# Optimization experiments

Measured on AMD Instinct MI355X. Metric: run time of the kernel, lower is better.

## Reference

```python
import jax, jax.numpy as jnp
import numpy as np

S, N, M, D = 4, 4096, 4096, 128
NEG = -1e30
EPS = 1e-12


def setup_inputs() -> dict:
    key = jax.random.key(0)
    k1, k2, k3 = jax.random.split(key, 3)
    art = jax.random.normal(k1, (S, N, D), dtype=jnp.float32)
    ref = jax.random.normal(k2, (S, M, D), dtype=jnp.float32)
    pos_mask = jax.random.randint(k3, (S, N, M), 0, 2).astype(jnp.bool_)
    log_temperature = jnp.log(jnp.asarray(0.01, dtype=jnp.float32))
    return {"art": art, "ref": ref, "pos_mask": pos_mask, "log_temperature": log_temperature}


def _l2norm(x):
    # F.normalize: x / max(||x||, eps)
    n = jnp.sqrt(jnp.sum(x * x, axis=-1, keepdims=True))
    return x / jnp.maximum(n, EPS)


def reference(art, ref, pos_mask, log_temperature):
    temp = jnp.exp(log_temperature)
    a = _l2norm(art)                                   # [S,N,D]
    r = _l2norm(ref)                                   # [S,M,D]
    logits = jnp.einsum("snd,smd->snm", a, r) / temp   # [S,N,M]

    den = jax.nn.logsumexp(logits, axis=-1)                              # [S,N]
    num = jax.nn.logsumexp(jnp.where(pos_mask, logits, NEG), axis=-1)    # [S,N]

    n_pos = jnp.sum(pos_mask, axis=-1)                 # [S,N]
    n_ref = logits.shape[-1]
    valid = (n_pos > 0) & (n_ref > n_pos)              # skip anchors with 0 pos or all pos

    per_anchor = den - num                             # -(num - den)
    cnt = jnp.sum(valid, axis=-1)                      # [S]
    stem_loss = jnp.sum(jnp.where(valid, per_anchor, 0.0), axis=-1) / jnp.maximum(cnt, 1)
    stem_valid = cnt > 0
    loss = jnp.sum(jnp.where(stem_valid, stem_loss, 0.0)) / jnp.maximum(jnp.sum(stem_valid), 1)
    return loss
```

## Files before the change

kernel.cpp:

```cpp
#include <hip/hip_runtime.h>
#include <hip/hip_bf16.h>
#include <math.h>

#define S_ 4
#define N_ 4096
#define M_ 4096
#define D_ 128
#define NEG_ (-1e30f)
#define CH_ 4
#define MCH_ (M_ / CH_)

typedef __bf16 bf16x8 __attribute__((ext_vector_type(8)));
typedef float f32x4 __attribute__((ext_vector_type(4)));

__device__ __forceinline__ unsigned short f2bf(float f) {
    unsigned u = __float_as_uint(f);
    unsigned r = (u + 0x7FFFu + ((u >> 16) & 1u)) >> 16;
    return (unsigned short)r;
}

__global__ void nrm_rows_kernel(const float* __restrict__ art, const float* __restrict__ ref,
                                unsigned short* __restrict__ an, unsigned short* __restrict__ rn) {
    const int w = threadIdx.x >> 6;
    const int lane = threadIdx.x & 63;
    const int row = blockIdx.x * 4 + w;
    const bool is_art = row < S_ * N_;
    const float* src = is_art ? (art + (size_t)row * D_)
                              : (ref + (size_t)(row - S_ * N_) * D_);
    unsigned short* dst = is_art ? (an + (size_t)row * D_)
                                 : (rn + (size_t)(row - S_ * N_) * D_);
    const float2 v = *reinterpret_cast<const float2*>(src + lane * 2);
    float ss = v.x * v.x + v.y * v.y;
#pragma unroll
    for (int off = 1; off < 64; off <<= 1) ss += __shfl_xor(ss, off);
    const float scale = 1.0f / fmaxf(sqrtf(ss), 1e-12f);
    unsigned pack = (unsigned)f2bf(v.x * scale) | ((unsigned)f2bf(v.y * scale) << 16);
    *reinterpret_cast<unsigned*>(dst + lane * 2) = pack;
}

__global__ __launch_bounds__(256, 6) void infonce_main_kernel(
    const unsigned short* __restrict__ an, const unsigned short* __restrict__ rn,
    const void* __restrict__ maskp, const float* __restrict__ logtemp,
    float4* __restrict__ part4, float* __restrict__ partn) {

    const int bid = blockIdx.x;
    const int swz = (bid & 7) * 256 + (bid >> 3);
    const int ch = swz >> 9;
    const int s = (swz >> 7) & 3;
    const int nblk = swz & 127;
    const int n_base = nblk * 32;

    const int tid = threadIdx.x;
    const int w = tid >> 6;
    const int lane = tid & 63;
    const int nsub = w & 1;
    const int msub = w >> 1;
    const int n16 = n_base + nsub * 16;
    const int lrow = lane & 15;
    const int lgrp = lane >> 4;
    const float inv_temp = __expf(-logtemp[0]);

    const unsigned probe = ((const unsigned*)maskp)[lane];
    const bool mask_is_byte = (__ballot(probe > 1u) != 0ull);

    bf16x8 bfr[4];
    const unsigned short* abase = an + ((size_t)(s * N_ + n16 + lrow)) * D_ + lgrp * 8;
#pragma unroll
    for (int kc = 0; kc < 4; ++kc)
        bfr[kc] = *reinterpret_cast<const bf16x8*>(abase + kc * 32);

    float dmax = NEG_, dsum = 0.f, nmax = NEG_, nsum = 0.f;
    int npos = 0;

    const int m_begin = ch * MCH_ + msub * (MCH_ / 2);
    const unsigned short* rbase = rn + ((size_t)(s * M_ + m_begin + lrow)) * D_ + lgrp * 8;
    const size_t mrow = ((size_t)(s * N_ + n16 + lrow)) * M_;

    for (int it = 0; it < (MCH_ / 2) / 32; ++it) {
        const int t0 = it * 2, t1 = t0 + 1;
        const int m0a = m_begin + t0 * 16 + lgrp * 4;
        const int m0b = m_begin + t1 * 16 + lgrp * 4;
        int pm[8];
        if (mask_is_byte) {
            const uchar4 ma = *reinterpret_cast<const uchar4*>((const unsigned char*)maskp + mrow + m0a);
            const uchar4 mb = *reinterpret_cast<const uchar4*>((const unsigned char*)maskp + mrow + m0b);
            pm[0] = ma.x; pm[1] = ma.y; pm[2] = ma.z; pm[3] = ma.w;
            pm[4] = mb.x; pm[5] = mb.y; pm[6] = mb.z; pm[7] = mb.w;
        } else {
            const int4 ma = *reinterpret_cast<const int4*>((const int*)maskp + mrow + m0a);
            const int4 mb = *reinterpret_cast<const int4*>((const int*)maskp + mrow + m0b);
            pm[0] = ma.x; pm[1] = ma.y; pm[2] = ma.z; pm[3] = ma.w;
            pm[4] = mb.x; pm[5] = mb.y; pm[6] = mb.z; pm[7] = mb.w;
        }
        f32x4 acc0 = {0.f, 0.f, 0.f, 0.f}, acc1 = {0.f, 0.f, 0.f, 0.f};
        const unsigned short* rp0 = rbase + (size_t)t0 * 16 * D_;
        const unsigned short* rp1 = rbase + (size_t)t1 * 16 * D_;
#pragma unroll
        for (int kc = 0; kc < 4; ++kc) {
            acc0 = __builtin_amdgcn_mfma_f32_16x16x32_bf16(
                *reinterpret_cast<const bf16x8*>(rp0 + kc * 32), bfr[kc], acc0, 0, 0, 0);
            acc1 = __builtin_amdgcn_mfma_f32_16x16x32_bf16(
                *reinterpret_cast<const bf16x8*>(rp1 + kc * 32), bfr[kc], acc1, 0, 0, 0);
        }
        float l[8];
#pragma unroll
        for (int i = 0; i < 4; ++i) { l[i] = acc0[i] * inv_temp; l[i + 4] = acc1[i] * inv_temp; }
        float tmax = fmaxf(fmaxf(fmaxf(l[0], l[1]), fmaxf(l[2], l[3])),
                           fmaxf(fmaxf(l[4], l[5]), fmaxf(l[6], l[7])));
        float nmx = fmaxf(dmax, tmax);
        float e = __expf(dmax - nmx) * dsum;
#pragma unroll
        for (int i = 0; i < 8; ++i) e += __expf(l[i] - nmx);
        dsum = e; dmax = nmx;
        float sm[8];
#pragma unroll
        for (int i = 0; i < 8; ++i) sm[i] = pm[i] ? l[i] : NEG_;
        float tmax2 = fmaxf(fmaxf(fmaxf(sm[0], sm[1]), fmaxf(sm[2], sm[3])),
                            fmaxf(fmaxf(sm[4], sm[5]), fmaxf(sm[6], sm[7])));
        float nmx2 = fmaxf(nmax, tmax2);
        float e2 = __expf(nmax - nmx2) * nsum;
#pragma unroll
        for (int i = 0; i < 8; ++i) e2 += __expf(sm[i] - nmx2);
        nsum = e2; nmax = nmx2;
#pragma unroll
        for (int i = 0; i < 8; ++i) npos += (pm[i] != 0);
    }

#pragma unroll
    for (int off = 16; off < 64; off <<= 1) {
        float odm = __shfl_xor(dmax, off), ods = __shfl_xor(dsum, off);
        float onm = __shfl_xor(nmax, off), ons = __shfl_xor(nsum, off);
        int onp = __shfl_xor(npos, off);
        float nm = fmaxf(dmax, odm);
        dsum = dsum * __expf(dmax - nm) + ods * __expf(odm - nm);
        dmax = nm;
        float nm2 = fmaxf(nmax, onm);
        nsum = nsum * __expf(nmax - nm2) + ons * __expf(onm - nm2);
        nmax = nm2;
        npos += onp;
    }

    __shared__ float lds[4][16][5];
    if (lane < 16) {
        lds[w][lane][0] = dmax; lds[w][lane][1] = dsum;
        lds[w][lane][2] = nmax; lds[w][lane][3] = nsum;
        lds[w][lane][4] = (float)npos;
    }
    __syncthreads();

    if (w == 0 && lane < 32) {
        const int wsub = lane >> 4;
        const int ni = lane & 15;
        float adm = lds[wsub][ni][0], ads = lds[wsub][ni][1];
        float anm = lds[wsub][ni][2], ans = lds[wsub][ni][3];
        float apc = lds[wsub][ni][4];
        float bdm = lds[wsub + 2][ni][0], bds = lds[wsub + 2][ni][1];
        float bnm = lds[wsub + 2][ni][2], bns = lds[wsub + 2][ni][3];
        float bpc = lds[wsub + 2][ni][4];
        float dm = fmaxf(adm, bdm);
        float ds = ads * __expf(adm - dm) + bds * __expf(bdm - dm);
        float nm = fmaxf(anm, bnm);
        float ns = ans * __expf(anm - nm) + bns * __expf(bnm - nm);
        const int ag = s * N_ + n_base + wsub * 16 + ni;
        part4[ag * CH_ + ch] = make_float4(dm, ds, nm, ns);
        partn[ag * CH_ + ch] = apc + bpc;
    }
}

__global__ void reduce_kernel(const float4* __restrict__ part4, const float* __restrict__ partn,
                              float* __restrict__ accum) {
    const int a = blockIdx.x * 256 + threadIdx.x;
    const int s = a >> 12;
    const int w = threadIdx.x >> 6;
    const int lane = threadIdx.x & 63;
    float dm = NEG_, ds = 0.f, nm = NEG_, ns = 0.f, np = 0.f;
#pragma unroll
    for (int ch = 0; ch < CH_; ++ch) {
        const float4 p = part4[a * CH_ + ch];
        const float pn = partn[a * CH_ + ch];
        float m2 = fmaxf(dm, p.x);
        ds = ds * __expf(dm - m2) + p.y * __expf(p.x - m2);
        dm = m2;
        float m3 = fmaxf(nm, p.z);
        ns = ns * __expf(nm - m3) + p.w * __expf(p.z - m3);
        nm = m3;
        np += pn;
    }
    const int npi = (int)np;
    const bool valid = (npi > 0) && (npi < M_);
    float pa = valid ? ((dm + __logf(ds)) - (nm + __logf(ns))) : 0.f;
    float cv = valid ? 1.f : 0.f;
#pragma unroll
    for (int off = 1; off < 64; off <<= 1) {
        pa += __shfl_xor(pa, off);
        cv += __shfl_xor(cv, off);
    }
    __shared__ float sp[4], sc[4];
    if (lane == 0) { sp[w] = pa; sc[w] = cv; }
    __syncthreads();
    if (threadIdx.x == 0) {
        atomicAdd(&accum[s * 2 + 0], sp[0] + sp[1] + sp[2] + sp[3]);
        atomicAdd(&accum[s * 2 + 1], sc[0] + sc[1] + sc[2] + sc[3]);
    }
}

__global__ void finalize_kernel(const float* __restrict__ accum, float* __restrict__ out) {
    if (threadIdx.x == 0) {
        float total = 0.f;
        int scnt = 0;
        for (int s = 0; s < S_; ++s) {
            float sum = accum[s * 2 + 0];
            float cnt = accum[s * 2 + 1];
            float stem = sum / fmaxf(cnt, 1.f);
            if (cnt > 0.f) { total += stem; scnt++; }
        }
        out[0] = total / (float)(scnt > 0 ? scnt : 1);
    }
}

extern "C" void kernel_launch(void* const* d_in, const int* in_sizes, int n_in,
                              void* d_out, int out_size, void* d_ws, size_t ws_size,
                              hipStream_t stream) {
    const float* art = (const float*)d_in[0];
    const float* ref = (const float*)d_in[1];
    const void* mask = d_in[2];
    const float* lt = (const float*)d_in[3];
    float* out = (float*)d_out;

    char* ws = (char*)d_ws;
    unsigned short* an = (unsigned short*)ws;
    unsigned short* rn = (unsigned short*)(ws + (size_t)4194304);
    float4* part4 = (float4*)(ws + (size_t)8388608);
    float* partn = (float*)(ws + (size_t)9437184);
    float* accum = (float*)(ws + (size_t)9699328);

    hipMemsetAsync(accum, 0, 2 * S_ * sizeof(float), stream);
    nrm_rows_kernel<<<(S_ * (N_ + M_)) / 4, 256, 0, stream>>>(art, ref, an, rn);
    infonce_main_kernel<<<S_ * (N_ / 32) * CH_, 256, 0, stream>>>(an, rn, mask, lt, part4, partn);
    reduce_kernel<<<(S_ * N_) / 256, 256, 0, stream>>>(part4, partn, accum);
    finalize_kernel<<<1, 64, 0, stream>>>(accum, out);
}
```

Measured before the change: 470.3 us.

## Share one running max for both log-sum-exps, use exp2 and mask-weighted sums

The main loop now keeps a single running max and rescale factor for both the denominator and the masked numerator. The numerator becomes a sum of mask-weighted exponentials in base 2, which halves the exp count and drops the second max and select chain. The loop is templated on mask type, processes 64 columns per iteration with four MFMAs in flight, and lowers the launch-bounds occupancy hint. The reduction path packs the count into the float4, removes the atomics and the memset, and does a deterministic block-partial finalize. The numerator can underflow to zero when all positive logits sit far below the overall max, which the old separate max avoided.

```diff
diff --git a/kernel.cpp b/kernel.cpp
--- a/kernel.cpp
+++ b/kernel.cpp
@@ -9,6 +9,8 @@
 #define NEG_ (-1e30f)
 #define CH_ 4
 #define MCH_ (M_ / CH_)
+#define LN2_ 0.69314718055994531f
+#define LOG2E_ 1.44269504088896340f
 
 typedef __bf16 bf16x8 __attribute__((ext_vector_type(8)));
 typedef float f32x4 __attribute__((ext_vector_type(4)));
@@ -38,10 +40,80 @@
     *reinterpret_cast<unsigned*>(dst + lane * 2) = pack;
 }
 
-__global__ __launch_bounds__(256, 6) void infonce_main_kernel(
+template <bool BYTE>
+__device__ __forceinline__ void lse_loop(
+    const unsigned short* __restrict__ rbase, const void* __restrict__ maskp,
+    size_t melt0, const bf16x8* __restrict__ bfr, float scale2,
+    float& dmax, float& dsum, float& nsum, float& npf) {
+#pragma unroll 2
+    for (int it = 0; it < (MCH_ / 2) / 64; ++it) {
+        float fpm[16];
+#pragma unroll
+        for (int t = 0; t < 4; ++t) {
+            if (BYTE) {
+                const uchar4 mv = *reinterpret_cast<const uchar4*>(
+                    (const unsigned char*)maskp + melt0 + it * 64 + t * 16);
+                fpm[t * 4 + 0] = (float)mv.x; fpm[t * 4 + 1] = (float)mv.y;
+                fpm[t * 4 + 2] = (float)mv.z; fpm[t * 4 + 3] = (float)mv.w;
+            } else {
+                const int4 mv = *reinterpret_cast<const int4*>(
+                    (const int*)maskp + melt0 + it * 64 + t * 16);
+                fpm[t * 4 + 0] = (float)mv.x; fpm[t * 4 + 1] = (float)mv.y;
+                fpm[t * 4 + 2] = (float)mv.z; fpm[t * 4 + 3] = (float)mv.w;
+            }
+        }
+        f32x4 acc0 = {0.f, 0.f, 0.f, 0.f}, acc1 = {0.f, 0.f, 0.f, 0.f};
+        f32x4 acc2 = {0.f, 0.f, 0.f, 0.f}, acc3 = {0.f, 0.f, 0.f, 0.f};
+        const unsigned short* rp = rbase + (size_t)it * 64 * D_;
+#pragma unroll
+        for (int kc = 0; kc < 4; ++kc) {
+            acc0 = __builtin_amdgcn_mfma_f32_16x16x32_bf16(
+                *reinterpret_cast<const bf16x8*>(rp + 0 * 16 * D_ + kc * 32), bfr[kc], acc0, 0, 0, 0);
+            acc1 = __builtin_amdgcn_mfma_f32_16x16x32_bf16(
+                *reinterpret_cast<const bf16x8*>(rp + 1 * 16 * D_ + kc * 32), bfr[kc], acc1, 0, 0, 0);
+            acc2 = __builtin_amdgcn_mfma_f32_16x16x32_bf16(
+                *reinterpret_cast<const bf16x8*>(rp + 2 * 16 * D_ + kc * 32), bfr[kc], acc2, 0, 0, 0);
+            acc3 = __builtin_amdgcn_mfma_f32_16x16x32_bf16(
+                *reinterpret_cast<const bf16x8*>(rp + 3 * 16 * D_ + kc * 32), bfr[kc], acc3, 0, 0, 0);
+        }
+        float l[16];
+#pragma unroll
+        for (int i = 0; i < 4; ++i) {
+            l[i]      = acc0[i] * scale2;  l[4 + i]  = acc1[i] * scale2;
+            l[8 + i]  = acc2[i] * scale2;  l[12 + i] = acc3[i] * scale2;
+        }
+        float a0 = fmaxf(l[0], l[1]),  a1 = fmaxf(l[2], l[3]);
+        float a2 = fmaxf(l[4], l[5]),  a3 = fmaxf(l[6], l[7]);
+        float a4 = fmaxf(l[8], l[9]),  a5 = fmaxf(l[10], l[11]);
+        float a6 = fmaxf(l[12], l[13]), a7 = fmaxf(l[14], l[15]);
+        float b0 = fmaxf(a0, a1), b1 = fmaxf(a2, a3), b2 = fmaxf(a4, a5), b3 = fmaxf(a6, a7);
+        float tmax = fmaxf(fmaxf(b0, b1), fmaxf(b2, b3));
+        const float nmx = fmaxf(dmax, tmax);
+        const float r = exp2f(dmax - nmx);
+        float e[16];
+#pragma unroll
+        for (int i = 0; i < 16; ++i) e[i] = exp2f(l[i] - nmx);
+        float s0 = (e[0] + e[1]) + (e[2] + e[3]), s1 = (e[4] + e[5]) + (e[6] + e[7]);
+        float s2 = (e[8] + e[9]) + (e[10] + e[11]), s3 = (e[12] + e[13]) + (e[14] + e[15]);
+        dsum = dsum * r + ((s0 + s1) + (s2 + s3));
+        float p0 = fpm[0] * e[0], p1 = fpm[1] * e[1], p2 = fpm[2] * e[2], p3 = fpm[3] * e[3];
+#pragma unroll
+        for (int i = 4; i < 16; i += 4) {
+            p0 = fmaf(fpm[i], e[i], p0);     p1 = fmaf(fpm[i + 1], e[i + 1], p1);
+            p2 = fmaf(fpm[i + 2], e[i + 2], p2); p3 = fmaf(fpm[i + 3], e[i + 3], p3);
+        }
+        nsum = nsum * r + ((p0 + p1) + (p2 + p3));
+        float q0 = (fpm[0] + fpm[1]) + (fpm[2] + fpm[3]), q1 = (fpm[4] + fpm[5]) + (fpm[6] + fpm[7]);
+        float q2 = (fpm[8] + fpm[9]) + (fpm[10] + fpm[11]), q3 = (fpm[12] + fpm[13]) + (fpm[14] + fpm[15]);
+        npf += ((q0 + q1) + (q2 + q3));
+        dmax = nmx;
+    }
+}
+
+__global__ __launch_bounds__(256, 4) void infonce_main_kernel(
     const unsigned short* __restrict__ an, const unsigned short* __restrict__ rn,
     const void* __restrict__ maskp, const float* __restrict__ logtemp,
-    float4* __restrict__ part4, float* __restrict__ partn) {
+    float4* __restrict__ part4) {
 
     const int bid = blockIdx.x;
     const int swz = (bid & 7) * 256 + (bid >> 3);
@@ -58,7 +130,7 @@
     const int n16 = n_base + nsub * 16;
     const int lrow = lane & 15;
     const int lgrp = lane >> 4;
-    const float inv_temp = __expf(-logtemp[0]);
+    const float scale2 = __expf(-logtemp[0]) * LOG2E_;
 
     const unsigned probe = ((const unsigned*)maskp)[lane];
     const bool mask_is_byte = (__ballot(probe > 1u) != 0ull);
@@ -69,126 +141,62 @@
     for (int kc = 0; kc < 4; ++kc)
         bfr[kc] = *reinterpret_cast<const bf16x8*>(abase + kc * 32);
 
-    float dmax = NEG_, dsum = 0.f, nmax = NEG_, nsum = 0.f;
-    int npos = 0;
-
     const int m_begin = ch * MCH_ + msub * (MCH_ / 2);
     const unsigned short* rbase = rn + ((size_t)(s * M_ + m_begin + lrow)) * D_ + lgrp * 8;
-    const size_t mrow = ((size_t)(s * N_ + n16 + lrow)) * M_;
-
-    for (int it = 0; it < (MCH_ / 2) / 32; ++it) {
-        const int t0 = it * 2, t1 = t0 + 1;
-        const int m0a = m_begin + t0 * 16 + lgrp * 4;
-        const int m0b = m_begin + t1 * 16 + lgrp * 4;
-        int pm[8];
-        if (mask_is_byte) {
-            const uchar4 ma = *reinterpret_cast<const uchar4*>((const unsigned char*)maskp + mrow + m0a);
-            const uchar4 mb = *reinterpret_cast<const uchar4*>((const unsigned char*)maskp + mrow + m0b);
-            pm[0] = ma.x; pm[1] = ma.y; pm[2] = ma.z; pm[3] = ma.w;
-            pm[4] = mb.x; pm[5] = mb.y; pm[6] = mb.z; pm[7] = mb.w;
-        } else {
-            const int4 ma = *reinterpret_cast<const int4*>((const int*)maskp + mrow + m0a);
-            const int4 mb = *reinterpret_cast<const int4*>((const int*)maskp + mrow + m0b);
-            pm[0] = ma.x; pm[1] = ma.y; pm[2] = ma.z; pm[3] = ma.w;
-            pm[4] = mb.x; pm[5] = mb.y; pm[6] = mb.z; pm[7] = mb.w;
-        }
-        f32x4 acc0 = {0.f, 0.f, 0.f, 0.f}, acc1 = {0.f, 0.f, 0.f, 0.f};
-        const unsigned short* rp0 = rbase + (size_t)t0 * 16 * D_;
-        const unsigned short* rp1 = rbase + (size_t)t1 * 16 * D_;
-#pragma unroll
-        for (int kc = 0; kc < 4; ++kc) {
-            acc0 = __builtin_amdgcn_mfma_f32_16x16x32_bf16(
-                *reinterpret_cast<const bf16x8*>(rp0 + kc * 32), bfr[kc], acc0, 0, 0, 0);
-            acc1 = __builtin_amdgcn_mfma_f32_16x16x32_bf16(
-                *reinterpret_cast<const bf16x8*>(rp1 + kc * 32), bfr[kc], acc1, 0, 0, 0);
-        }
-        float l[8];
-#pragma unroll
-        for (int i = 0; i < 4; ++i) { l[i] = acc0[i] * inv_temp; l[i + 4] = acc1[i] * inv_temp; }
-        float tmax = fmaxf(fmaxf(fmaxf(l[0], l[1]), fmaxf(l[2], l[3])),
-                           fmaxf(fmaxf(l[4], l[5]), fmaxf(l[6], l[7])));
-        float nmx = fmaxf(dmax, tmax);
-        float e = __expf(dmax - nmx) * dsum;
-#pragma unroll
-        for (int i = 0; i < 8; ++i) e += __expf(l[i] - nmx);
-        dsum = e; dmax = nmx;
-        float sm[8];
-#pragma unroll
-        for (int i = 0; i < 8; ++i) sm[i] = pm[i] ? l[i] : NEG_;
-        float tmax2 = fmaxf(fmaxf(fmaxf(sm[0], sm[1]), fmaxf(sm[2], sm[3])),
-                            fmaxf(fmaxf(sm[4], sm[5]), fmaxf(sm[6], sm[7])));
-        float nmx2 = fmaxf(nmax, tmax2);
-        float e2 = __expf(nmax - nmx2) * nsum;
-#pragma unroll
-        for (int i = 0; i < 8; ++i) e2 += __expf(sm[i] - nmx2);
-        nsum = e2; nmax = nmx2;
-#pragma unroll
-        for (int i = 0; i < 8; ++i) npos += (pm[i] != 0);
-    }
+    const size_t melt0 = ((size_t)(s * N_ + n16 + lrow)) * M_ + m_begin + lgrp * 4;
+
+    float dmax = NEG_, dsum = 0.f, nsum = 0.f, npf = 0.f;
+    if (mask_is_byte) lse_loop<true >(rbase, maskp, melt0, bfr, scale2, dmax, dsum, nsum, npf);
+    else              lse_loop<false>(rbase, maskp, melt0, bfr, scale2, dmax, dsum, nsum, npf);
 
 #pragma unroll
     for (int off = 16; off < 64; off <<= 1) {
         float odm = __shfl_xor(dmax, off), ods = __shfl_xor(dsum, off);
-        float onm = __shfl_xor(nmax, off), ons = __shfl_xor(nsum, off);
-        int onp = __shfl_xor(npos, off);
+        float ons = __shfl_xor(nsum, off), onp = __shfl_xor(npf, off);
         float nm = fmaxf(dmax, odm);
-        dsum = dsum * __expf(dmax - nm) + ods * __expf(odm - nm);
+        float ra = exp2f(dmax - nm), rb = exp2f(odm - nm);
+        dsum = dsum * ra + ods * rb;
+        nsum = nsum * ra + ons * rb;
+        npf += onp;
         dmax = nm;
-        float nm2 = fmaxf(nmax, onm);
-        nsum = nsum * __expf(nmax - nm2) + ons * __expf(onm - nm2);
-        nmax = nm2;
-        npos += onp;
-    }
-
-    __shared__ float lds[4][16][5];
-    if (lane < 16) {
-        lds[w][lane][0] = dmax; lds[w][lane][1] = dsum;
-        lds[w][lane][2] = nmax; lds[w][lane][3] = nsum;
-        lds[w][lane][4] = (float)npos;
-    }
+    }
+
+    __shared__ float4 lds4[4][16];
+    if (lane < 16) lds4[w][lane] = make_float4(dmax, dsum, nsum, npf);
     __syncthreads();
 
     if (w == 0 && lane < 32) {
         const int wsub = lane >> 4;
         const int ni = lane & 15;
-        float adm = lds[wsub][ni][0], ads = lds[wsub][ni][1];
-        float anm = lds[wsub][ni][2], ans = lds[wsub][ni][3];
-        float apc = lds[wsub][ni][4];
-        float bdm = lds[wsub + 2][ni][0], bds = lds[wsub + 2][ni][1];
-        float bnm = lds[wsub + 2][ni][2], bns = lds[wsub + 2][ni][3];
-        float bpc = lds[wsub + 2][ni][4];
-        float dm = fmaxf(adm, bdm);
-        float ds = ads * __expf(adm - dm) + bds * __expf(bdm - dm);
-        float nm = fmaxf(anm, bnm);
-        float ns = ans * __expf(anm - nm) + bns * __expf(bnm - nm);
+        const float4 A = lds4[wsub][ni];
+        const float4 B = lds4[wsub + 2][ni];
+        const float nm = fmaxf(A.x, B.x);
+        const float ra = exp2f(A.x - nm), rb = exp2f(B.x - nm);
+        const float ds = A.y * ra + B.y * rb;
+        const float ns = A.z * ra + B.z * rb;
+        const float np = A.w + B.w;
         const int ag = s * N_ + n_base + wsub * 16 + ni;
-        part4[ag * CH_ + ch] = make_float4(dm, ds, nm, ns);
-        partn[ag * CH_ + ch] = apc + bpc;
-    }
-}
-
-__global__ void reduce_kernel(const float4* __restrict__ part4, const float* __restrict__ partn,
-                              float* __restrict__ accum) {
+        part4[ag * CH_ + ch] = make_float4(nm, ds, ns, np);
+    }
+}
+
+__global__ void reduce_kernel(const float4* __restrict__ part4, float2* __restrict__ bpart) {
     const int a = blockIdx.x * 256 + threadIdx.x;
-    const int s = a >> 12;
     const int w = threadIdx.x >> 6;
     const int lane = threadIdx.x & 63;
-    float dm = NEG_, ds = 0.f, nm = NEG_, ns = 0.f, np = 0.f;
+    float dm = NEG_, ds = 0.f, ns = 0.f, npf = 0.f;
 #pragma unroll
     for (int ch = 0; ch < CH_; ++ch) {
         const float4 p = part4[a * CH_ + ch];
-        const float pn = partn[a * CH_ + ch];
-        float m2 = fmaxf(dm, p.x);
-        ds = ds * __expf(dm - m2) + p.y * __expf(p.x - m2);
+        const float m2 = fmaxf(dm, p.x);
+        const float ra = exp2f(dm - m2), rb = exp2f(p.x - m2);
+        ds = ds * ra + p.y * rb;
+        ns = ns * ra + p.z * rb;
+        npf += p.w;
         dm = m2;
-        float m3 = fmaxf(nm, p.z);
-        ns = ns * __expf(nm - m3) + p.w * __expf(p.z - m3);
-        nm = m3;
-        np += pn;
-    }
-    const int npi = (int)np;
-    const bool valid = (npi > 0) && (npi < M_);
-    float pa = valid ? ((dm + __logf(ds)) - (nm + __logf(ns))) : 0.f;
+    }
+    const bool valid = (npf > 0.5f) && (npf < (float)M_ - 0.5f);
+    float pa = valid ? LN2_ * (log2f(ds) - log2f(ns)) : 0.f;
     float cv = valid ? 1.f : 0.f;
 #pragma unroll
     for (int off = 1; off < 64; off <<= 1) {
@@ -198,21 +206,32 @@
     __shared__ float sp[4], sc[4];
     if (lane == 0) { sp[w] = pa; sc[w] = cv; }
     __syncthreads();
-    if (threadIdx.x == 0) {
-        atomicAdd(&accum[s * 2 + 0], sp[0] + sp[1] + sp[2] + sp[3]);
-        atomicAdd(&accum[s * 2 + 1], sc[0] + sc[1] + sc[2] + sc[3]);
-    }
-}
-
-__global__ void finalize_kernel(const float* __restrict__ accum, float* __restrict__ out) {
-    if (threadIdx.x == 0) {
+    if (threadIdx.x == 0)
+        bpart[blockIdx.x] = make_float2(sp[0] + sp[1] + sp[2] + sp[3],
+                                        sc[0] + sc[1] + sc[2] + sc[3]);
+}
+
+__global__ void finalize_kernel(const float2* __restrict__ bpart, float* __restrict__ out) {
+    const int t = threadIdx.x;
+    const float2 v = bpart[t];
+    float pa = v.x, cv = v.y;
+#pragma unroll
+    for (int off = 1; off < 16; off <<= 1) {
+        pa += __shfl_xor(pa, off);
+        cv += __shfl_xor(cv, off);
+    }
+    const float p0 = __shfl(pa, 0),  c0 = __shfl(cv, 0);
+    const float p1 = __shfl(pa, 16), c1 = __shfl(cv, 16);
+    const float p2 = __shfl(pa, 32), c2 = __shfl(cv, 32);
+    const float p3 = __shfl(pa, 48), c3 = __shfl(cv, 48);
+    if (t == 0) {
         float total = 0.f;
         int scnt = 0;
+        const float ps[4] = {p0, p1, p2, p3};
+        const float cs[4] = {c0, c1, c2, c3};
         for (int s = 0; s < S_; ++s) {
-            float sum = accum[s * 2 + 0];
-            float cnt = accum[s * 2 + 1];
-            float stem = sum / fmaxf(cnt, 1.f);
-            if (cnt > 0.f) { total += stem; scnt++; }
+            const float stem = ps[s] / fmaxf(cs[s], 1.f);
+            if (cs[s] > 0.f) { total += stem; scnt++; }
         }
         out[0] = total / (float)(scnt > 0 ? scnt : 1);
     }
@@ -231,12 +250,10 @@
     unsigned short* an = (unsigned short*)ws;
     unsigned short* rn = (unsigned short*)(ws + (size_t)4194304);
     float4* part4 = (float4*)(ws + (size_t)8388608);
-    float* partn = (float*)(ws + (size_t)9437184);
-    float* accum = (float*)(ws + (size_t)9699328);
-
-    hipMemsetAsync(accum, 0, 2 * S_ * sizeof(float), stream);
+    float2* bpart = (float2*)(ws + (size_t)9437184);
+
     nrm_rows_kernel<<<(S_ * (N_ + M_)) / 4, 256, 0, stream>>>(art, ref, an, rn);
-    infonce_main_kernel<<<S_ * (N_ / 32) * CH_, 256, 0, stream>>>(an, rn, mask, lt, part4, partn);
-    reduce_kernel<<<(S_ * N_) / 256, 256, 0, stream>>>(part4, partn, accum);
-    finalize_kernel<<<1, 64, 0, stream>>>(accum, out);
-}
+    infonce_main_kernel<<<S_ * (N_ / 32) * CH_, 256, 0, stream>>>(an, rn, mask, lt, part4);
+    reduce_kernel<<<(S_ * N_) / 256, 256, 0, stream>>>(part4, bpart);
+    finalize_kernel<<<1, 64, 0, stream>>>(bpart, out);
+}
```

Measured after the change: 461.2 us. No clear change (-1.9%).
